# Kernel tuning notes

Hardware: AMD Instinct MI355X
Metric: run time of the kernel (lower is better)

## Reference

```python
import jax, jax.numpy as jnp
import numpy as np
import math

D_MODEL = 1024
N_HEADS = 16
SLOT_DIM = 64
N_SLOTS = 1024
TOP_K = 2
LN_EPS = 1e-5


def setup_inputs() -> dict:
    key = jax.random.key(0)
    ks = jax.random.split(key, 8)
    x = jax.random.normal(ks[0], (4, 2048, D_MODEL), dtype=jnp.float32)
    ln_gamma = jnp.ones((D_MODEL,), jnp.float32)
    ln_beta = jnp.zeros((D_MODEL,), jnp.float32)
    q_w = jax.random.normal(ks[1], (N_HEADS * SLOT_DIM, D_MODEL), jnp.float32) / math.sqrt(D_MODEL)
    q_b = jnp.zeros((N_HEADS * SLOT_DIM,), jnp.float32)
    slot_signatures = jax.random.normal(ks[2], (N_HEADS, N_SLOTS, SLOT_DIM), jnp.float32) * 0.5
    slot_values = jax.random.normal(ks[3], (N_HEADS, N_SLOTS, SLOT_DIM), jnp.float32) * 0.02
    out_w = jax.random.normal(ks[4], (D_MODEL, N_HEADS * SLOT_DIM), jnp.float32) / math.sqrt(N_HEADS * SLOT_DIM)
    out_b = jnp.zeros((D_MODEL,), jnp.float32)
    temperature = jnp.ones((1,), jnp.float32)
    return {"x": x, "ln_gamma": ln_gamma, "ln_beta": ln_beta, "q_w": q_w, "q_b": q_b,
            "slot_signatures": slot_signatures, "slot_values": slot_values,
            "out_w": out_w, "out_b": out_b, "temperature": temperature}


def _ternary_ste(sig):
    # forward = {-1,0,+1} quantization; backward = identity (straight-through)
    q = jnp.where(sig > 0.3, 1.0, jnp.where(sig < -0.3, -1.0, 0.0))
    return sig + jax.lax.stop_gradient(q - sig)


def reference(x, ln_gamma, ln_beta, q_w, q_b, slot_signatures, slot_values, out_w, out_b, temperature):
    B, T, D = x.shape
    # LayerNorm
    mean = jnp.mean(x, axis=-1, keepdims=True)
    var = jnp.var(x, axis=-1, keepdims=True)
    x_norm = (x - mean) * jax.lax.rsqrt(var + LN_EPS) * ln_gamma + ln_beta
    # Query projection -> [B, T, H, slot_dim]
    q = (x_norm @ q_w.T + q_b).reshape(B, T, N_HEADS, SLOT_DIM)
    sigs = _ternary_ste(slot_signatures)  # [H, S, d]
    scores = jnp.einsum('bthd,hsd->bths', q, sigs)
    scores = scores / (temperature * math.sqrt(SLOT_DIM))  # [B, T, H, S]
    # top-k routing
    topk_scores, slot_idx = jax.lax.top_k(scores, TOP_K)  # [B, T, H, K]
    weights = jax.nn.softmax(topk_scores, axis=-1)
    # gather selected slot values: [B, T, H, K, d]
    h_idx = jnp.arange(N_HEADS)[None, None, :, None]
    selected = slot_values[h_idx, slot_idx]
    read = jnp.sum(selected * weights[..., None], axis=3)  # [B, T, H, d]
    read = read.reshape(B, T, N_HEADS * SLOT_DIM)
    out = read @ out_w.T + out_b
    return x + out
```

## Files before the change

### kernel.cpp

```cpp
#include <hip/hip_runtime.h>

typedef unsigned short u16;
typedef unsigned int   u32;
typedef float f32x4  __attribute__((ext_vector_type(4)));
typedef float f32x16 __attribute__((ext_vector_type(16)));
typedef __bf16 bf16x8 __attribute__((ext_vector_type(8)));

__device__ __forceinline__ u16 f2bf(float f){
  u32 u = __float_as_uint(f);
  u += 0x7fffu + ((u >> 16) & 1u);
  return (u16)(u >> 16);
}

__device__ __forceinline__ void gld16(const void* g, void* l){
  __builtin_amdgcn_global_load_lds((const __attribute__((address_space(1))) u32*)g,
                                   (__attribute__((address_space(3))) u32*)l, 16, 0, 0);
}

__global__ __launch_bounds__(256) void convert_kernel(
    const float* __restrict__ qw, const float* __restrict__ ow,
    const float* __restrict__ sg,
    u16* __restrict__ qwb, u16* __restrict__ owb, u16* __restrict__ sgb){
  int i = blockIdx.x * 256 + threadIdx.x;
  qwb[i] = f2bf(qw[i]);
  owb[i] = f2bf(ow[i]);
  float s = sg[i];
  float t = (s > 0.3f) ? 1.0f : ((s < -0.3f) ? -1.0f : 0.0f);
  sgb[i] = f2bf(t);
}

__global__ __launch_bounds__(256) void ln_kernel(
    const float* __restrict__ x, const float* __restrict__ g,
    const float* __restrict__ b, u16* __restrict__ xn){
  const int t = blockIdx.x, tid = threadIdx.x;
  f32x4 v = *(const f32x4*)(x + (size_t)t * 1024 + tid * 4);
  float s  = v[0] + v[1] + v[2] + v[3];
  float ss = v[0]*v[0] + v[1]*v[1] + v[2]*v[2] + v[3]*v[3];
  for (int off = 32; off; off >>= 1){
    s  += __shfl_down(s, off);
    ss += __shfl_down(ss, off);
  }
  __shared__ float red[8];
  int w = tid >> 6;
  if ((tid & 63) == 0){ red[w] = s; red[4 + w] = ss; }
  __syncthreads();
  s  = red[0] + red[1] + red[2] + red[3];
  ss = red[4] + red[5] + red[6] + red[7];
  float mean = s * (1.0f / 1024.0f);
  float var  = ss * (1.0f / 1024.0f) - mean * mean;
  float rs   = rsqrtf(var + 1e-5f);
  f32x4 gv = *(const f32x4*)(g + tid * 4);
  f32x4 bv = *(const f32x4*)(b + tid * 4);
  float y0 = (v[0]-mean)*rs*gv[0]+bv[0];
  float y1 = (v[1]-mean)*rs*gv[1]+bv[1];
  float y2 = (v[2]-mean)*rs*gv[2]+bv[2];
  float y3 = (v[3]-mean)*rs*gv[3]+bv[3];
  uint2 pk;
  pk.x = (u32)f2bf(y0) | ((u32)f2bf(y1) << 16);
  pk.y = (u32)f2bf(y2) | ((u32)f2bf(y3) << 16);
  *(uint2*)(xn + (size_t)t * 1024 + tid * 4) = pk;
}

__global__ __launch_bounds__(256, 3) void gemm_bt(
    const u16* __restrict__ A, const u16* __restrict__ B,
    const float* __restrict__ bias, const float* __restrict__ resid,
    float* __restrict__ outf, u16* __restrict__ outb, int mode){
  __shared__ u16 As[128 * 64];
  __shared__ u16 Bs[128 * 64];
  const int tid = threadIdx.x;
  const int m0 = blockIdx.y * 128, n0 = blockIdx.x * 128;
  const int w = tid >> 6, lane = tid & 63, lm = lane & 15, quad = lane >> 4;
  const int wm = (w & 1) * 64, wn = (w >> 1) * 64;
  const int lr = lane >> 3;
  const int lg = (lane & 7) ^ lr;
  const f32x4 fz = {0.f, 0.f, 0.f, 0.f};
  f32x4 acc[4][4];
  #pragma unroll
  for (int i = 0; i < 4; ++i)
    #pragma unroll
    for (int j = 0; j < 4; ++j) acc[i][j] = fz;

  const u16* gA = A + (size_t)(m0 + w * 32 + lr) * 1024 + lg * 8;
  const u16* gB = B + (size_t)(n0 + w * 32 + lr) * 1024 + lg * 8;
  u16* lA = &As[(w * 32) * 64];
  u16* lB = &Bs[(w * 32) * 64];
  const int sw = lm & 7;

  for (int kt = 0; kt < 16; ++kt){
    #pragma unroll
    for (int sub = 0; sub < 4; ++sub){
      gld16(gA + (size_t)(sub * 8) * 1024 + kt * 64, lA + sub * 8 * 64);
      gld16(gB + (size_t)(sub * 8) * 1024 + kt * 64, lB + sub * 8 * 64);
    }
    __syncthreads();
    #pragma unroll
    for (int kk = 0; kk < 2; ++kk){
      const int ch = ((quad + kk * 4) ^ sw) * 8;
      bf16x8 afr[4], bfr[4];
      #pragma unroll
      for (int i = 0; i < 4; ++i)
        afr[i] = *(const bf16x8*)(&As[(wm + i * 16 + lm) * 64 + ch]);
      #pragma unroll
      for (int j = 0; j < 4; ++j)
        bfr[j] = *(const bf16x8*)(&Bs[(wn + j * 16 + lm) * 64 + ch]);
      #pragma unroll
      for (int i = 0; i < 4; ++i)
        #pragma unroll
        for (int j = 0; j < 4; ++j)
          acc[i][j] = __builtin_amdgcn_mfma_f32_16x16x32_bf16(afr[i], bfr[j], acc[i][j], 0, 0, 0);
    }
    __syncthreads();
  }

  #pragma unroll
  for (int i = 0; i < 4; ++i){
    #pragma unroll
    for (int r = 0; r < 4; ++r){
      int grow = m0 + wm + i * 16 + quad * 4 + r;
      #pragma unroll
      for (int j = 0; j < 4; ++j){
        int gcol = n0 + wn + j * 16 + lm;
        float v = acc[i][j][r] + bias[gcol];
        if (mode){
          v += resid[(size_t)grow * 1024 + gcol];
          outf[(size_t)grow * 1024 + gcol] = v;
        } else {
          outb[(size_t)grow * 1024 + gcol] = f2bf(v);
        }
      }
    }
  }
}

__global__ __launch_bounds__(256, 4) void route_kernel(
    const u16* __restrict__ q, const u16* __restrict__ sig,
    const float* __restrict__ V, const float* __restrict__ temp,
    u16* __restrict__ rd){
  const int h = blockIdx.y;
  const int t0 = blockIdx.x * 128;
  const int tid = threadIdx.x, w = tid >> 6, lane = tid & 63;
  const int col = lane & 31, half = lane >> 5;

  __shared__ u16 sbuf[2][128 * 64];
  __shared__ float fw1[128], fw2[128];
  __shared__ int   fi1[128], fi2[128];

  const u16* qrow = q + (size_t)(t0 + w * 32 + col) * 1024 + h * 64 + half * 8;
  bf16x8 afr[4];
  #pragma unroll
  for (int c = 0; c < 4; ++c) afr[c] = *(const bf16x8*)(qrow + c * 16);

  const u16* sigh = sig + (size_t)h * 65536;

  const int lr = lane >> 3, lg = (lane & 7) ^ lr;
  const u16* ssrc = sigh + (size_t)(w * 32 + lr) * 64 + lg * 8;
  auto stage = [&](int t, int b){
    const u16* s0 = ssrc + (size_t)t * 128 * 64;
    u16* d0 = &sbuf[b][(w * 32) * 64];
    #pragma unroll
    for (int sub = 0; sub < 4; ++sub)
      gld16(s0 + sub * 8 * 64, d0 + sub * 8 * 64);
  };

  int p0 = ((0 + half) ^ (col & 7)) * 8;
  int p1 = ((2 + half) ^ (col & 7)) * 8;
  int p2 = ((4 + half) ^ (col & 7)) * 8;
  int p3 = ((6 + half) ^ (col & 7)) * 8;

  const f32x16 fzero = {};
  float v1[16], v2[16];
  #pragma unroll
  for (int r = 0; r < 16; ++r){ v1[r] = -3.0e38f; v2[r] = -3.0e38f; }

  stage(0, 0);
  for (int t = 0; t < 8; ++t){
    __syncthreads();
    if (t < 7) stage(t + 1, (t + 1) & 1);
    const u16* buf = sbuf[t & 1];
    #pragma unroll
    for (int sbl = 0; sbl < 4; ++sbl){
      const u16* srow = &buf[(sbl * 32 + col) * 64];
      bf16x8 b0 = *(const bf16x8*)(srow + p0);
      bf16x8 b1 = *(const bf16x8*)(srow + p1);
      bf16x8 b2 = *(const bf16x8*)(srow + p2);
      bf16x8 b3 = *(const bf16x8*)(srow + p3);
      f32x16 acc;
      acc = __builtin_amdgcn_mfma_f32_32x32x16_bf16(afr[0], b0, fzero, 0, 0, 0);
      acc = __builtin_amdgcn_mfma_f32_32x32x16_bf16(afr[1], b1, acc, 0, 0, 0);
      acc = __builtin_amdgcn_mfma_f32_32x32x16_bf16(afr[2], b2, acc, 0, 0, 0);
      acc = __builtin_amdgcn_mfma_f32_32x32x16_bf16(afr[3], b3, acc, 0, 0, 0);
      u32 sidx = (u32)(t * 128 + sbl * 32 + col);
      #pragma unroll
      for (int r = 0; r < 16; ++r){
        u32 u = __float_as_uint(acc[r]);
        float key = __uint_as_float((u & 0xFFFFFC00u) | sidx);
        float o1 = v1[r];
        v1[r] = fmaxf(o1, key);
        v2[r] = __builtin_amdgcn_fmed3f(o1, v2[r], key);
      }
    }
  }

  #pragma unroll
  for (int off = 1; off < 32; off <<= 1){
    #pragma unroll
    for (int r = 0; r < 16; ++r){
      float b1v = __shfl_xor(v1[r], off);
      float b2v = __shfl_xor(v2[r], off);
      float a1 = v1[r];
      v1[r] = fmaxf(a1, b1v);
      v2[r] = __builtin_amdgcn_fmed3f(a1, b1v, fmaxf(v2[r], b2v));
    }
  }

  if (col == 0){
    float tsc = 1.0f / (temp[0] * 8.0f);
    #pragma unroll
    for (int r = 0; r < 16; ++r){
      int row = (r & 3) + 8 * (r >> 2) + 4 * half;
      int tl = w * 32 + row;
      u32 u1 = __float_as_uint(v1[r]);
      u32 u2 = __float_as_uint(v2[r]);
      float s1 = __uint_as_float(u1 & 0xFFFFFC00u);
      float s2 = __uint_as_float(u2 & 0xFFFFFC00u);
      float ex = __expf((s2 - s1) * tsc);
      float iw = 1.0f / (1.0f + ex);
      fw1[tl] = iw; fw2[tl] = ex * iw;
      fi1[tl] = (int)(u1 & 1023u); fi2[tl] = (int)(u2 & 1023u);
    }
  }
  __syncthreads();

  int tl = tid >> 1, d0 = (tid & 1) * 32;
  const float* va = V + ((size_t)h * 1024 + fi1[tl]) * 64 + d0;
  const float* vb = V + ((size_t)h * 1024 + fi2[tl]) * 64 + d0;
  float W1 = fw1[tl], W2 = fw2[tl];
  u16* dst = rd + (size_t)(t0 + tl) * 1024 + h * 64 + d0;
  #pragma unroll
  for (int g = 0; g < 4; ++g){
    f32x4 xa = *(const f32x4*)(va + g * 8);
    f32x4 xb = *(const f32x4*)(va + g * 8 + 4);
    f32x4 ya = *(const f32x4*)(vb + g * 8);
    f32x4 yb = *(const f32x4*)(vb + g * 8 + 4);
    uint4 o;
    o.x = (u32)f2bf(W1*xa[0]+W2*ya[0]) | ((u32)f2bf(W1*xa[1]+W2*ya[1]) << 16);
    o.y = (u32)f2bf(W1*xa[2]+W2*ya[2]) | ((u32)f2bf(W1*xa[3]+W2*ya[3]) << 16);
    o.z = (u32)f2bf(W1*xb[0]+W2*yb[0]) | ((u32)f2bf(W1*xb[1]+W2*yb[1]) << 16);
    o.w = (u32)f2bf(W1*xb[2]+W2*yb[2]) | ((u32)f2bf(W1*xb[3]+W2*yb[3]) << 16);
    *(uint4*)(dst + g * 8) = o;
  }
}

extern "C" void kernel_launch(void* const* d_in, const int* in_sizes, int n_in,
                              void* d_out, int out_size, void* d_ws, size_t ws_size,
                              hipStream_t stream){
  const float* x    = (const float*)d_in[0];
  const float* lng  = (const float*)d_in[1];
  const float* lnb  = (const float*)d_in[2];
  const float* qw   = (const float*)d_in[3];
  const float* qb   = (const float*)d_in[4];
  const float* sig  = (const float*)d_in[5];
  const float* sv   = (const float*)d_in[6];
  const float* ow   = (const float*)d_in[7];
  const float* ob   = (const float*)d_in[8];
  const float* temp = (const float*)d_in[9];
  float* out = (float*)d_out;

  char* ws = (char*)d_ws;
  u16* xn   = (u16*)(ws);
  u16* qwb  = (u16*)(ws + 16777216);
  u16* owb  = (u16*)(ws + 16777216 + 2097152);
  u16* sgb  = (u16*)(ws + 16777216 + 2 * 2097152);
  u16* qb16 = (u16*)(ws + 16777216 + 3 * 2097152);
  u16* rdb  = xn;

  convert_kernel<<<4096, 256, 0, stream>>>(qw, ow, sig, qwb, owb, sgb);
  ln_kernel<<<8192, 256, 0, stream>>>(x, lng, lnb, xn);
  gemm_bt<<<dim3(8, 64), 256, 0, stream>>>(xn, qwb, qb, nullptr, nullptr, qb16, 0);
  route_kernel<<<dim3(64, 16), 256, 0, stream>>>(qb16, sgb, sv, temp, rdb);
  gemm_bt<<<dim3(8, 64), 256, 0, stream>>>(rdb, owb, ob, x, out, nullptr, 1);
}
```

Before: 217.6 us.

## Remap GEMM block order, halve-and-distribute route top-2 merge, relax occupancy

The GEMM grid becomes a flat 1D launch whose block index is remapped, so consecutive blocks walk M-tiles spread across XCD-sized groups while sharing the same N tile, aiming for better L2 locality. In the route kernel, the butterfly top-2 reduction over 16 rows now halves the live register set each shuffle round, spreading the results across lanes. This cuts shuffle and ALU work from 16x5 rounds to 16+8+4+2+1, and the final softmax and index writes now run in 16 lanes in parallel instead of one lane looping. The route kernel's launch bounds are also changed to waves_per_eu(2,4), which gives the compiler more register freedom at the possible cost of occupancy.

After: 217.4 us. Within noise of the previous version (-0.1%).

```diff
diff --git a/kernel.cpp b/kernel.cpp
--- a/kernel.cpp
+++ b/kernel.cpp
@@ -68,7 +68,9 @@
   __shared__ u16 As[128 * 64];
   __shared__ u16 Bs[128 * 64];
   const int tid = threadIdx.x;
-  const int m0 = blockIdx.y * 128, n0 = blockIdx.x * 128;
+  const int b = blockIdx.x;
+  const int m0 = ((b & 7) * 8 + ((b >> 3) & 7)) * 128;
+  const int n0 = (b >> 6) * 128;
   const int w = tid >> 6, lane = tid & 63, lm = lane & 15, quad = lane >> 4;
   const int wm = (w & 1) * 64, wn = (w >> 1) * 64;
   const int lr = lane >> 3;
@@ -132,7 +134,28 @@
   }
 }
 
-__global__ __launch_bounds__(256, 4) void route_kernel(
+template<int O, int L>
+__device__ __forceinline__ void merge_round(float* v1, float* v2, int col){
+  float t1[L], t2[L];
+  #pragma unroll
+  for (int i = 0; i < L; ++i){ t1[i] = __shfl_xor(v1[i], O); t2[i] = __shfl_xor(v2[i], O); }
+  if constexpr (L > 1){
+    const int s = (col & O) ? L / 2 : 0;
+    #pragma unroll
+    for (int i = 0; i < L / 2; ++i){
+      float m1 = v1[s + i], m2 = v2[s + i], o1 = t1[s + i], o2 = t2[s + i];
+      v1[i] = fmaxf(m1, o1);
+      v2[i] = __builtin_amdgcn_fmed3f(m1, o1, fmaxf(m2, o2));
+    }
+  } else {
+    float m1 = v1[0];
+    v1[0] = fmaxf(m1, t1[0]);
+    v2[0] = __builtin_amdgcn_fmed3f(m1, t1[0], fmaxf(v2[0], t2[0]));
+  }
+}
+
+__global__ __launch_bounds__(256) __attribute__((amdgpu_waves_per_eu(2, 4)))
+void route_kernel(
     const u16* __restrict__ q, const u16* __restrict__ sig,
     const float* __restrict__ V, const float* __restrict__ temp,
     u16* __restrict__ rd){
@@ -154,9 +177,9 @@
 
   const int lr = lane >> 3, lg = (lane & 7) ^ lr;
   const u16* ssrc = sigh + (size_t)(w * 32 + lr) * 64 + lg * 8;
-  auto stage = [&](int t, int b){
+  auto stage = [&](int t, int bb){
     const u16* s0 = ssrc + (size_t)t * 128 * 64;
-    u16* d0 = &sbuf[b][(w * 32) * 64];
+    u16* d0 = &sbuf[bb][(w * 32) * 64];
     #pragma unroll
     for (int sub = 0; sub < 4; ++sub)
       gld16(s0 + sub * 8 * 64, d0 + sub * 8 * 64);
@@ -201,33 +224,25 @@
     }
   }
 
-  #pragma unroll
-  for (int off = 1; off < 32; off <<= 1){
-    #pragma unroll
-    for (int r = 0; r < 16; ++r){
-      float b1v = __shfl_xor(v1[r], off);
-      float b2v = __shfl_xor(v2[r], off);
-      float a1 = v1[r];
-      v1[r] = fmaxf(a1, b1v);
-      v2[r] = __builtin_amdgcn_fmed3f(a1, b1v, fmaxf(v2[r], b2v));
-    }
-  }
-
-  if (col == 0){
-    float tsc = 1.0f / (temp[0] * 8.0f);
-    #pragma unroll
-    for (int r = 0; r < 16; ++r){
-      int row = (r & 3) + 8 * (r >> 2) + 4 * half;
-      int tl = w * 32 + row;
-      u32 u1 = __float_as_uint(v1[r]);
-      u32 u2 = __float_as_uint(v2[r]);
-      float s1 = __uint_as_float(u1 & 0xFFFFFC00u);
-      float s2 = __uint_as_float(u2 & 0xFFFFFC00u);
-      float ex = __expf((s2 - s1) * tsc);
-      float iw = 1.0f / (1.0f + ex);
-      fw1[tl] = iw; fw2[tl] = ex * iw;
-      fi1[tl] = (int)(u1 & 1023u); fi2[tl] = (int)(u2 & 1023u);
-    }
+  merge_round<16, 16>(v1, v2, col);
+  merge_round< 8,  8>(v1, v2, col);
+  merge_round< 4,  4>(v1, v2, col);
+  merge_round< 2,  2>(v1, v2, col);
+  merge_round< 1,  1>(v1, v2, col);
+
+  float tsc = 1.0f / (temp[0] * 8.0f);
+  if ((col & 1) == 0){
+    int r = (col >> 1) & 15;
+    int row = (r & 3) + 8 * (r >> 2) + 4 * half;
+    int tl = w * 32 + row;
+    u32 u1 = __float_as_uint(v1[0]);
+    u32 u2 = __float_as_uint(v2[0]);
+    float s1 = __uint_as_float(u1 & 0xFFFFFC00u);
+    float s2 = __uint_as_float(u2 & 0xFFFFFC00u);
+    float ex = __expf((s2 - s1) * tsc);
+    float iw = 1.0f / (1.0f + ex);
+    fw1[tl] = iw; fw2[tl] = ex * iw;
+    fi1[tl] = (int)(u1 & 1023u); fi2[tl] = (int)(u2 & 1023u);
   }
   __syncthreads();
 
@@ -276,7 +291,7 @@
 
   convert_kernel<<<4096, 256, 0, stream>>>(qw, ow, sig, qwb, owb, sgb);
   ln_kernel<<<8192, 256, 0, stream>>>(x, lng, lnb, xn);
-  gemm_bt<<<dim3(8, 64), 256, 0, stream>>>(xn, qwb, qb, nullptr, nullptr, qb16, 0);
+  gemm_bt<<<512, 256, 0, stream>>>(xn, qwb, qb, nullptr, nullptr, qb16, 0);
   route_kernel<<<dim3(64, 16), 256, 0, stream>>>(qb16, sgb, sv, temp, rdb);
-  gemm_bt<<<dim3(8, 64), 256, 0, stream>>>(rdb, owb, ob, x, out, nullptr, 1);
-}
+  gemm_bt<<<512, 256, 0, stream>>>(rdb, owb, ob, x, out, nullptr, 1);
+}
```

## Restructure routing top-2 with transposed MFMA, vectorize convert, remap GEMM block order

Applied to the files above, without the earlier changes.

The routing kernel now swaps the MFMA operands so each lane holds the 16 slot scores of one token. It reduces those 16 scores to a top-2 in registers with a max/median tree and tracks the 32-slot block index separately. This replaces the per-row running top-2 over 16 rows and the 5-stage cross-lane shuffle reduction with a single xor-32 merge, at the cost of packing only 5 low index bits into the score. The convert kernel is vectorized to 4 elements per thread, and the GEMM launch is flattened to 1D with a remapped block order meant to improve cache reuse of B tiles. The occupancy hint on the route kernel is also dropped.

Result: faster. 211.7 us (-2.7%).

```diff
diff --git a/kernel.cpp b/kernel.cpp
--- a/kernel.cpp
+++ b/kernel.cpp
@@ -21,12 +21,24 @@
     const float* __restrict__ qw, const float* __restrict__ ow,
     const float* __restrict__ sg,
     u16* __restrict__ qwb, u16* __restrict__ owb, u16* __restrict__ sgb){
-  int i = blockIdx.x * 256 + threadIdx.x;
-  qwb[i] = f2bf(qw[i]);
-  owb[i] = f2bf(ow[i]);
-  float s = sg[i];
-  float t = (s > 0.3f) ? 1.0f : ((s < -0.3f) ? -1.0f : 0.0f);
-  sgb[i] = f2bf(t);
+  int i = (blockIdx.x * 256 + threadIdx.x) * 4;
+  f32x4 a = *(const f32x4*)(qw + i);
+  f32x4 b = *(const f32x4*)(ow + i);
+  f32x4 s = *(const f32x4*)(sg + i);
+  uint2 pa, pb, ps;
+  pa.x = (u32)f2bf(a[0]) | ((u32)f2bf(a[1]) << 16);
+  pa.y = (u32)f2bf(a[2]) | ((u32)f2bf(a[3]) << 16);
+  pb.x = (u32)f2bf(b[0]) | ((u32)f2bf(b[1]) << 16);
+  pb.y = (u32)f2bf(b[2]) | ((u32)f2bf(b[3]) << 16);
+  float t0 = (s[0] > 0.3f) ? 1.0f : ((s[0] < -0.3f) ? -1.0f : 0.0f);
+  float t1 = (s[1] > 0.3f) ? 1.0f : ((s[1] < -0.3f) ? -1.0f : 0.0f);
+  float t2 = (s[2] > 0.3f) ? 1.0f : ((s[2] < -0.3f) ? -1.0f : 0.0f);
+  float t3 = (s[3] > 0.3f) ? 1.0f : ((s[3] < -0.3f) ? -1.0f : 0.0f);
+  ps.x = (u32)f2bf(t0) | ((u32)f2bf(t1) << 16);
+  ps.y = (u32)f2bf(t2) | ((u32)f2bf(t3) << 16);
+  *(uint2*)(qwb + i) = pa;
+  *(uint2*)(owb + i) = pb;
+  *(uint2*)(sgb + i) = ps;
 }
 
 __global__ __launch_bounds__(256) void ln_kernel(
@@ -68,7 +80,9 @@
   __shared__ u16 As[128 * 64];
   __shared__ u16 Bs[128 * 64];
   const int tid = threadIdx.x;
-  const int m0 = blockIdx.y * 128, n0 = blockIdx.x * 128;
+  const int b = blockIdx.x;
+  const int m0 = ((b & 7) * 8 + ((b >> 3) & 7)) * 128;
+  const int n0 = (b >> 6) * 128;
   const int w = tid >> 6, lane = tid & 63, lm = lane & 15, quad = lane >> 4;
   const int wm = (w & 1) * 64, wn = (w >> 1) * 64;
   const int lr = lane >> 3;
@@ -132,7 +146,7 @@
   }
 }
 
-__global__ __launch_bounds__(256, 4) void route_kernel(
+__global__ __launch_bounds__(256) void route_kernel(
     const u16* __restrict__ q, const u16* __restrict__ sig,
     const float* __restrict__ V, const float* __restrict__ temp,
     u16* __restrict__ rd){
@@ -154,9 +168,9 @@
 
   const int lr = lane >> 3, lg = (lane & 7) ^ lr;
   const u16* ssrc = sigh + (size_t)(w * 32 + lr) * 64 + lg * 8;
-  auto stage = [&](int t, int b){
+  auto stage = [&](int t, int bb){
     const u16* s0 = ssrc + (size_t)t * 128 * 64;
-    u16* d0 = &sbuf[b][(w * 32) * 64];
+    u16* d0 = &sbuf[bb][(w * 32) * 64];
     #pragma unroll
     for (int sub = 0; sub < 4; ++sub)
       gld16(s0 + sub * 8 * 64, d0 + sub * 8 * 64);
@@ -167,10 +181,13 @@
   int p2 = ((4 + half) ^ (col & 7)) * 8;
   int p3 = ((6 + half) ^ (col & 7)) * 8;
 
+  u32 rk[16];
+  #pragma unroll
+  for (int r = 0; r < 16; ++r) rk[r] = (u32)((r & 3) + 8 * (r >> 2) + 4 * half);
+
   const f32x16 fzero = {};
-  float v1[16], v2[16];
-  #pragma unroll
-  for (int r = 0; r < 16; ++r){ v1[r] = -3.0e38f; v2[r] = -3.0e38f; }
+  float v1 = -3.0e38f, v2 = -3.0e38f;
+  u32 b1 = 0, b2 = 0;
 
   stage(0, 0);
   for (int t = 0; t < 8; ++t){
@@ -180,54 +197,76 @@
     #pragma unroll
     for (int sbl = 0; sbl < 4; ++sbl){
       const u16* srow = &buf[(sbl * 32 + col) * 64];
-      bf16x8 b0 = *(const bf16x8*)(srow + p0);
-      bf16x8 b1 = *(const bf16x8*)(srow + p1);
-      bf16x8 b2 = *(const bf16x8*)(srow + p2);
-      bf16x8 b3 = *(const bf16x8*)(srow + p3);
+      bf16x8 s0 = *(const bf16x8*)(srow + p0);
+      bf16x8 s1 = *(const bf16x8*)(srow + p1);
+      bf16x8 s2 = *(const bf16x8*)(srow + p2);
+      bf16x8 s3 = *(const bf16x8*)(srow + p3);
       f32x16 acc;
-      acc = __builtin_amdgcn_mfma_f32_32x32x16_bf16(afr[0], b0, fzero, 0, 0, 0);
-      acc = __builtin_amdgcn_mfma_f32_32x32x16_bf16(afr[1], b1, acc, 0, 0, 0);
-      acc = __builtin_amdgcn_mfma_f32_32x32x16_bf16(afr[2], b2, acc, 0, 0, 0);
-      acc = __builtin_amdgcn_mfma_f32_32x32x16_bf16(afr[3], b3, acc, 0, 0, 0);
-      u32 sidx = (u32)(t * 128 + sbl * 32 + col);
-      #pragma unroll
-      for (int r = 0; r < 16; ++r){
-        u32 u = __float_as_uint(acc[r]);
-        float key = __uint_as_float((u & 0xFFFFFC00u) | sidx);
-        float o1 = v1[r];
-        v1[r] = fmaxf(o1, key);
-        v2[r] = __builtin_amdgcn_fmed3f(o1, v2[r], key);
+      acc = __builtin_amdgcn_mfma_f32_32x32x16_bf16(s0, afr[0], fzero, 0, 0, 0);
+      acc = __builtin_amdgcn_mfma_f32_32x32x16_bf16(s1, afr[1], acc, 0, 0, 0);
+      acc = __builtin_amdgcn_mfma_f32_32x32x16_bf16(s2, afr[2], acc, 0, 0, 0);
+      acc = __builtin_amdgcn_mfma_f32_32x32x16_bf16(s3, afr[3], acc, 0, 0, 0);
+      float k[16];
+      #pragma unroll
+      for (int r = 0; r < 16; ++r)
+        k[r] = __uint_as_float((__float_as_uint(acc[r]) & 0xFFFFFFE0u) | rk[r]);
+      float h1[8], h2[8];
+      #pragma unroll
+      for (int i = 0; i < 8; ++i){
+        h1[i] = fmaxf(k[2*i], k[2*i+1]);
+        h2[i] = fminf(k[2*i], k[2*i+1]);
       }
+      float g1[4], g2[4];
+      #pragma unroll
+      for (int i = 0; i < 4; ++i){
+        g1[i] = fmaxf(h1[2*i], h1[2*i+1]);
+        g2[i] = __builtin_amdgcn_fmed3f(h1[2*i], h1[2*i+1], fmaxf(h2[2*i], h2[2*i+1]));
+      }
+      float e1[2], e2[2];
+      #pragma unroll
+      for (int i = 0; i < 2; ++i){
+        e1[i] = fmaxf(g1[2*i], g1[2*i+1]);
+        e2[i] = __builtin_amdgcn_fmed3f(g1[2*i], g1[2*i+1], fmaxf(g2[2*i], g2[2*i+1]));
+      }
+      float m1 = fmaxf(e1[0], e1[1]);
+      float m2 = __builtin_amdgcn_fmed3f(e1[0], e1[1], fmaxf(e2[0], e2[1]));
+      u32 bt = (u32)(t * 4 + sbl);
+      u32   cb2 = (m2 > v2) ? bt : b2;
+      float c2  = fmaxf(v2, m2);
+      u32   nb1 = (m1 > v1) ? bt : b1;
+      float n1  = fmaxf(v1, m1);
+      float n2  = __builtin_amdgcn_fmed3f(v1, m1, c2);
+      u32   nb2 = (n2 == m1) ? bt : ((n2 == v1) ? b1 : cb2);
+      v1 = n1; b1 = nb1; v2 = n2; b2 = nb2;
     }
   }
 
-  #pragma unroll
-  for (int off = 1; off < 32; off <<= 1){
-    #pragma unroll
-    for (int r = 0; r < 16; ++r){
-      float b1v = __shfl_xor(v1[r], off);
-      float b2v = __shfl_xor(v2[r], off);
-      float a1 = v1[r];
-      v1[r] = fmaxf(a1, b1v);
-      v2[r] = __builtin_amdgcn_fmed3f(a1, b1v, fmaxf(v2[r], b2v));
-    }
-  }
-
-  if (col == 0){
+  {
+    float o1 = __shfl_xor(v1, 32);
+    float o2 = __shfl_xor(v2, 32);
+    u32 ob1 = (u32)__shfl_xor((int)b1, 32);
+    u32 ob2 = (u32)__shfl_xor((int)b2, 32);
+    u32   cb2 = (o2 > v2) ? ob2 : b2;
+    float c2  = fmaxf(v2, o2);
+    u32   nb1 = (o1 > v1) ? ob1 : b1;
+    float n1  = fmaxf(v1, o1);
+    float n2  = __builtin_amdgcn_fmed3f(v1, o1, c2);
+    u32   nb2 = (n2 == o1) ? ob1 : ((n2 == v1) ? b1 : cb2);
+    v1 = n1; b1 = nb1; v2 = n2; b2 = nb2;
+  }
+
+  if (half == 0){
+    int tl = w * 32 + col;
+    u32 u1 = __float_as_uint(v1);
+    u32 u2 = __float_as_uint(v2);
+    float s1 = __uint_as_float(u1 & 0xFFFFFFE0u);
+    float s2 = __uint_as_float(u2 & 0xFFFFFFE0u);
     float tsc = 1.0f / (temp[0] * 8.0f);
-    #pragma unroll
-    for (int r = 0; r < 16; ++r){
-      int row = (r & 3) + 8 * (r >> 2) + 4 * half;
-      int tl = w * 32 + row;
-      u32 u1 = __float_as_uint(v1[r]);
-      u32 u2 = __float_as_uint(v2[r]);
-      float s1 = __uint_as_float(u1 & 0xFFFFFC00u);
-      float s2 = __uint_as_float(u2 & 0xFFFFFC00u);
-      float ex = __expf((s2 - s1) * tsc);
-      float iw = 1.0f / (1.0f + ex);
-      fw1[tl] = iw; fw2[tl] = ex * iw;
-      fi1[tl] = (int)(u1 & 1023u); fi2[tl] = (int)(u2 & 1023u);
-    }
+    float ex = __expf((s2 - s1) * tsc);
+    float iw = 1.0f / (1.0f + ex);
+    fw1[tl] = iw; fw2[tl] = ex * iw;
+    fi1[tl] = (int)(b1 * 32 + (u1 & 31u));
+    fi2[tl] = (int)(b2 * 32 + (u2 & 31u));
   }
   __syncthreads();
 
@@ -274,9 +313,9 @@
   u16* qb16 = (u16*)(ws + 16777216 + 3 * 2097152);
   u16* rdb  = xn;
 
-  convert_kernel<<<4096, 256, 0, stream>>>(qw, ow, sig, qwb, owb, sgb);
+  convert_kernel<<<1024, 256, 0, stream>>>(qw, ow, sig, qwb, owb, sgb);
   ln_kernel<<<8192, 256, 0, stream>>>(x, lng, lnb, xn);
-  gemm_bt<<<dim3(8, 64), 256, 0, stream>>>(xn, qwb, qb, nullptr, nullptr, qb16, 0);
+  gemm_bt<<<512, 256, 0, stream>>>(xn, qwb, qb, nullptr, nullptr, qb16, 0);
   route_kernel<<<dim3(64, 16), 256, 0, stream>>>(qb16, sgb, sv, temp, rdb);
-  gemm_bt<<<dim3(8, 64), 256, 0, stream>>>(rdb, owb, ob, x, out, nullptr, 1);
-}
+  gemm_bt<<<512, 256, 0, stream>>>(rdb, owb, ob, x, out, nullptr, 1);
+}
```
